# Optimization experiments

Measured on AMD Instinct MI355X. Metric: run time of the kernel, lower is better.

## Reference

```python
import jax, jax.numpy as jnp
import numpy as np

POOL_H, POOL_W = 7, 7
SCALE = 0.25
SAMPLING = 2  # fixed sampling ratio (static grid)


def _sample_coords(lo, bin_sz, pool, s):
    # lo: [N], bin_sz: [N] -> coords [N, pool*s]
    # point iy within bin: (iy + 0.5) / s of a bin
    offs = (jnp.arange(pool)[:, None] + (jnp.arange(s)[None, :] + 0.5) / s).reshape(-1)  # [pool*s]
    return lo[:, None] + offs[None, :] * bin_sz[:, None]


def roi_align(feat, rois, roibatches):
    B, C, H, W = feat.shape
    N = rois.shape[0]
    x1 = rois[:, 0] * SCALE
    y1 = rois[:, 1] * SCALE
    x2 = rois[:, 2] * SCALE
    y2 = rois[:, 3] * SCALE
    roi_w = jnp.maximum(x2 - x1, 1.0)
    roi_h = jnp.maximum(y2 - y1, 1.0)
    bin_w = roi_w / POOL_W
    bin_h = roi_h / POOL_H

    ys = _sample_coords(y1, bin_h, POOL_H, SAMPLING)  # [N, Gy]
    xs = _sample_coords(x1, bin_w, POOL_W, SAMPLING)  # [N, Gx]
    Gy, Gx = ys.shape[1], xs.shape[1]

    vy = (ys >= -1.0) & (ys <= H)  # out-of-range samples contribute 0
    vx = (xs >= -1.0) & (xs <= W)

    yc = jnp.clip(ys, 0.0, H - 1)
    xc = jnp.clip(xs, 0.0, W - 1)
    y_lo = jnp.clip(jnp.floor(yc).astype(jnp.int32), 0, H - 1)
    x_lo = jnp.clip(jnp.floor(xc).astype(jnp.int32), 0, W - 1)
    y_hi = jnp.minimum(y_lo + 1, H - 1)
    x_hi = jnp.minimum(x_lo + 1, W - 1)
    ly = yc - y_lo  # [N, Gy]
    lx = xc - x_lo  # [N, Gx]
    hy = 1.0 - ly
    hx = 1.0 - lx

    b = roibatches.astype(jnp.int32)[:, None, None]  # [N,1,1]

    def gather(yi, xi):
        # advanced indexing -> [N, Gy, Gx, C]
        return feat[b, :, yi[:, :, None], xi[:, None, :]]

    v_ll = gather(y_lo, x_lo)
    v_lh = gather(y_lo, x_hi)
    v_hl = gather(y_hi, x_lo)
    v_hh = gather(y_hi, x_hi)

    wy_l = (hy * vy)[:, :, None, None]
    wy_h = (ly * vy)[:, :, None, None]
    wx_l = (hx * vx)[:, None, :, None]
    wx_h = (lx * vx)[:, None, :, None]

    vals = (wy_l * wx_l * v_ll + wy_l * wx_h * v_lh
            + wy_h * wx_l * v_hl + wy_h * wx_h * v_hh)  # [N, Gy, Gx, C]

    # average pool over the SAMPLING x SAMPLING points per bin
    vals = vals.reshape(N, POOL_H, SAMPLING, POOL_W, SAMPLING, C)
    out = vals.mean(axis=(2, 4))  # [N, POOL_H, POOL_W, C]
    return jnp.transpose(out, (0, 3, 1, 2))  # [N, C, POOL_H, POOL_W]


def setup_inputs() -> dict:
    key = jax.random.key(0)
    k1, k2, k3, k4 = jax.random.split(key, 4)
    B, C, H, W = 4, 256, 200, 304
    N = 1024
    img_h, img_w = H / SCALE, W / SCALE
    feat = jax.random.normal(k1, (B, C, H, W), dtype=jnp.float32)
    xa = jax.random.uniform(k2, (N, 2), minval=0.0, maxval=img_w)
    ya = jax.random.uniform(k3, (N, 2), minval=0.0, maxval=img_h)
    rois = jnp.stack([xa.min(1), ya.min(1), xa.max(1), ya.max(1)], axis=1).astype(jnp.float32)
    roibatches = jax.random.randint(k4, (N,), 0, B, dtype=jnp.int32)
    return {"feat": feat, "rois": rois, "roibatches": roibatches}


def reference(feat, rois, roibatches):
    return roi_align(feat, rois, roibatches)
```

## Files before the change

kernel.cpp:

```cpp
#include <hip/hip_runtime.h>
#include <hip/hip_bf16.h>


#define POOL 7
constexpr int Bc = 4;
constexpr int Cc = 256;
constexpr int Hc = 200;
constexpr int Wc = 304;
constexpr int HWc = Hc * Wc;
constexpr float SCALEc = 0.25f;

static __device__ __forceinline__ float bf16_lo(unsigned u) {
    u <<= 16;
    return __builtin_bit_cast(float, u);
}
static __device__ __forceinline__ float bf16_hi(unsigned u) {
    u &= 0xFFFF0000u;
    return __builtin_bit_cast(float, u);
}

__global__ __launch_bounds__(256) void nchw_to_nhwc_bf16(
    const float* __restrict__ in, ushort* __restrict__ outp)
{
    __shared__ float tile[128][65];
    int b  = blockIdx.z;
    int p0 = blockIdx.x * 64;
    int c0 = blockIdx.y * 128;
    int tx = threadIdx.x;
    int ty = threadIdx.y;

    const float* src = in + ((size_t)b * Cc + c0) * (size_t)HWc + p0;
#pragma unroll
    for (int k = 0; k < 32; ++k) {
        int c = ty + 4 * k;
        tile[c][tx] = src[(size_t)c * HWc + tx];
    }
    __syncthreads();

#pragma unroll
    for (int k = 0; k < 16; ++k) {
        int p = ty + 4 * k;
        float f0 = tile[2 * tx][p];
        float f1 = tile[2 * tx + 1][p];
        unsigned u0 = (unsigned)__hip_bfloat16_raw(__float2bfloat16(f0)).x;
        unsigned u1 = (unsigned)__hip_bfloat16_raw(__float2bfloat16(f1)).x;
        unsigned packed = u0 | (u1 << 16);
        size_t d = ((size_t)b * HWc + p0 + p) * (size_t)Cc + c0 + 2 * tx;
        *(unsigned*)(outp + d) = packed;
    }
}

__global__ __launch_bounds__(256) void roialign_gather(
    const ushort* __restrict__ f,
    const float*  __restrict__ rois,
    const int*    __restrict__ rb,
    float*        __restrict__ out)
{
    __shared__ float stage[49 * 257];

    int n    = blockIdx.x;
    int t    = threadIdx.x;
    int wav  = t >> 6;
    int lane = t & 63;
    int half = lane >> 5;
    int sub  = lane & 31;

    float x1 = rois[n * 4 + 0] * SCALEc;
    float y1 = rois[n * 4 + 1] * SCALEc;
    float x2 = rois[n * 4 + 2] * SCALEc;
    float y2 = rois[n * 4 + 3] * SCALEc;
    int   b  = rb[n];

    float roi_w = fmaxf(x2 - x1, 1.0f);
    float roi_h = fmaxf(y2 - y1, 1.0f);
    float bin_w = roi_w * (1.0f / POOL);
    float bin_h = roi_h * (1.0f / POOL);

    const ushort* base = f + (size_t)b * ((size_t)HWc * Cc) + (size_t)sub * 8;

#pragma unroll 1
    for (int it = 0; it < 7; ++it) {
        int bin = it * 8 + wav * 2 + half;
        if (bin < 49) {
            int ph = bin / POOL;
            int pw = bin % POOL;

            int   yy[2][2];  float wy[2][2];
#pragma unroll
            for (int iy = 0; iy < 2; ++iy) {
                float y  = y1 + ((float)ph + ((float)iy + 0.5f) * 0.5f) * bin_h;
                bool  vy = (y >= -1.0f) && (y <= (float)Hc);
                float yc = fminf(fmaxf(y, 0.0f), (float)(Hc - 1));
                int   y_lo = (int)floorf(yc);
                int   y_hi = min(y_lo + 1, Hc - 1);
                float ly = yc - (float)y_lo;
                yy[iy][0] = y_lo;  yy[iy][1] = y_hi;
                wy[iy][0] = vy ? (1.0f - ly) : 0.0f;
                wy[iy][1] = vy ? ly : 0.0f;
            }
            int   xx[2][2];  float wx[2][2];
#pragma unroll
            for (int ix = 0; ix < 2; ++ix) {
                float x  = x1 + ((float)pw + ((float)ix + 0.5f) * 0.5f) * bin_w;
                bool  vx = (x >= -1.0f) && (x <= (float)Wc);
                float xc = fminf(fmaxf(x, 0.0f), (float)(Wc - 1));
                int   x_lo = (int)floorf(xc);
                int   x_hi = min(x_lo + 1, Wc - 1);
                float lx = xc - (float)x_lo;
                xx[ix][0] = x_lo;  xx[ix][1] = x_hi;
                wx[ix][0] = vx ? (1.0f - lx) : 0.0f;
                wx[ix][1] = vx ? lx : 0.0f;
            }

            float acc[8] = {0.f, 0.f, 0.f, 0.f, 0.f, 0.f, 0.f, 0.f};
#pragma unroll
            for (int iy = 0; iy < 2; ++iy) {
#pragma unroll
                for (int yl = 0; yl < 2; ++yl) {
                    const ushort* row = base + (size_t)yy[iy][yl] * ((size_t)Wc * Cc);
                    float wyv = wy[iy][yl];
#pragma unroll
                    for (int ix = 0; ix < 2; ++ix) {
#pragma unroll
                        for (int xl = 0; xl < 2; ++xl) {
                            float w = wyv * wx[ix][xl];
                            const uint4 v = *(const uint4*)(row + (size_t)xx[ix][xl] * Cc);
                            acc[0] = fmaf(w, bf16_lo(v.x), acc[0]);
                            acc[1] = fmaf(w, bf16_hi(v.x), acc[1]);
                            acc[2] = fmaf(w, bf16_lo(v.y), acc[2]);
                            acc[3] = fmaf(w, bf16_hi(v.y), acc[3]);
                            acc[4] = fmaf(w, bf16_lo(v.z), acc[4]);
                            acc[5] = fmaf(w, bf16_hi(v.z), acc[5]);
                            acc[6] = fmaf(w, bf16_lo(v.w), acc[6]);
                            acc[7] = fmaf(w, bf16_hi(v.w), acc[7]);
                        }
                    }
                }
            }
            float* sp = &stage[bin * 257 + sub * 8];
#pragma unroll
            for (int j = 0; j < 8; ++j) sp[j] = acc[j] * 0.25f;
        }
    }
    __syncthreads();

    float* obase = out + (size_t)n * (Cc * POOL * POOL);
#pragma unroll 1
    for (int k = 0; k < 49; ++k) {
        int flat = t + 256 * k;
        int c    = flat / 49;
        int bin  = flat - c * 49;
        obase[flat] = stage[bin * 257 + c];
    }
}

__global__ __launch_bounds__(256) void roialign_fwd(
    const float* __restrict__ feat,
    const float* __restrict__ rois,
    const int* __restrict__ roibatches,
    float* __restrict__ out,
    int total)
{
    int tid = blockIdx.x * blockDim.x + threadIdx.x;
    if (tid >= total) return;
    int n   = tid / (Cc * POOL * POOL);
    int rem = tid % (Cc * POOL * POOL);
    int c   = rem / (POOL * POOL);
    int bin = rem % (POOL * POOL);
    int ph  = bin / POOL;
    int pw  = bin % POOL;

    float x1 = rois[n * 4 + 0] * SCALEc;
    float y1 = rois[n * 4 + 1] * SCALEc;
    float x2 = rois[n * 4 + 2] * SCALEc;
    float y2 = rois[n * 4 + 3] * SCALEc;
    int   b  = roibatches[n];

    float roi_w = fmaxf(x2 - x1, 1.0f);
    float roi_h = fmaxf(y2 - y1, 1.0f);
    float bin_w = roi_w * (1.0f / POOL);
    float bin_h = roi_h * (1.0f / POOL);

    const float* fp = feat + (size_t)(b * Cc + c) * (size_t)HWc;

    float acc = 0.0f;
#pragma unroll
    for (int iy = 0; iy < 2; ++iy) {
        float y  = y1 + ((float)ph + ((float)iy + 0.5f) * 0.5f) * bin_h;
        bool  vy = (y >= -1.0f) && (y <= (float)Hc);
        float yc = fminf(fmaxf(y, 0.0f), (float)(Hc - 1));
        int   y_lo = (int)floorf(yc);
        int   y_hi = min(y_lo + 1, Hc - 1);
        float ly = yc - (float)y_lo;
        float hy = 1.0f - ly;
        float wyl = vy ? hy : 0.0f;
        float wyh = vy ? ly : 0.0f;
        const float* row_lo = fp + (size_t)y_lo * Wc;
        const float* row_hi = fp + (size_t)y_hi * Wc;
#pragma unroll
        for (int ix = 0; ix < 2; ++ix) {
            float x  = x1 + ((float)pw + ((float)ix + 0.5f) * 0.5f) * bin_w;
            bool  vx = (x >= -1.0f) && (x <= (float)Wc);
            float xc = fminf(fmaxf(x, 0.0f), (float)(Wc - 1));
            int   x_lo = (int)floorf(xc);
            int   x_hi = min(x_lo + 1, Wc - 1);
            float lx = xc - (float)x_lo;
            float hx = 1.0f - lx;
            float wxl = vx ? hx : 0.0f;
            float wxh = vx ? lx : 0.0f;
            acc += wyl * (wxl * row_lo[x_lo] + wxh * row_lo[x_hi])
                 + wyh * (wxl * row_hi[x_lo] + wxh * row_hi[x_hi]);
        }
    }
    out[tid] = acc * 0.25f;
}

extern "C" void kernel_launch(void* const* d_in, const int* in_sizes, int n_in,
                              void* d_out, int out_size, void* d_ws, size_t ws_size,
                              hipStream_t stream)
{
    const float* feat       = (const float*)d_in[0];
    const float* rois       = (const float*)d_in[1];
    const int*   roibatches = (const int*)d_in[2];
    float*       out        = (float*)d_out;
    int N = in_sizes[1] / 4;

    size_t need = (size_t)Bc * HWc * Cc * sizeof(ushort);
    if (ws_size >= need) {
        ushort* fbh = (ushort*)d_ws;
        dim3 tgrid(HWc / 64, Cc / 128, Bc);
        dim3 tblock(64, 4);
        nchw_to_nhwc_bf16<<<tgrid, tblock, 0, stream>>>(feat, fbh);

        roialign_gather<<<N, 256, 0, stream>>>(fbh, rois, roibatches, out);
    } else {
        int total = out_size;
        roialign_fwd<<<(total + 255) / 256, 256, 0, stream>>>(
            feat, rois, roibatches, out, total);
    }
}
```

Measured before the change: 129.4 us.

## Vectorize NHWC transpose stores, double gather block size, batch gather loads

The transpose kernel now writes 16-byte uint4 stores of eight packed bf16 channels instead of 4-byte stores, with an XOR swizzle on the shared tile to limit bank conflicts on the new read pattern. The gather kernel launches 512 threads per ROI so each wave handles fewer bins, and it issues all eight row loads for a sample row before the FMAs to expose more memory-level parallelism. The cost is more registers held per thread and a bounds check in the output copy loop.

```diff
diff --git a/kernel.cpp b/kernel.cpp
--- a/kernel.cpp
+++ b/kernel.cpp
@@ -18,6 +18,11 @@
     u &= 0xFFFF0000u;
     return __builtin_bit_cast(float, u);
 }
+static __device__ __forceinline__ unsigned pack_bf16(float f0, float f1) {
+    unsigned u0 = (unsigned)__hip_bfloat16_raw(__float2bfloat16(f0)).x;
+    unsigned u1 = (unsigned)__hip_bfloat16_raw(__float2bfloat16(f1)).x;
+    return u0 | (u1 << 16);
+}
 
 __global__ __launch_bounds__(256) void nchw_to_nhwc_bf16(
     const float* __restrict__ in, ushort* __restrict__ outp)
@@ -33,24 +38,31 @@
 #pragma unroll
     for (int k = 0; k < 32; ++k) {
         int c = ty + 4 * k;
-        tile[c][tx] = src[(size_t)c * HWc + tx];
+        tile[c][tx ^ ((c >> 5) & 3)] = src[(size_t)c * HWc + tx];
     }
     __syncthreads();
 
-#pragma unroll
-    for (int k = 0; k < 16; ++k) {
-        int p = ty + 4 * k;
-        float f0 = tile[2 * tx][p];
-        float f1 = tile[2 * tx + 1][p];
-        unsigned u0 = (unsigned)__hip_bfloat16_raw(__float2bfloat16(f0)).x;
-        unsigned u1 = (unsigned)__hip_bfloat16_raw(__float2bfloat16(f1)).x;
-        unsigned packed = u0 | (u1 << 16);
-        size_t d = ((size_t)b * HWc + p0 + p) * (size_t)Cc + c0 + 2 * tx;
-        *(unsigned*)(outp + d) = packed;
-    }
-}
-
-__global__ __launch_bounds__(256) void roialign_gather(
+    int t  = ty * 64 + tx;
+    int cg = t & 15;
+    int pi = t >> 4;
+#pragma unroll
+    for (int k = 0; k < 4; ++k) {
+        int p = pi + 16 * k;
+        unsigned u[4];
+#pragma unroll
+        for (int j = 0; j < 4; ++j) {
+            int ce = cg * 8 + 2 * j;
+            int co = ce + 1;
+            float f0 = tile[ce][p ^ ((ce >> 5) & 3)];
+            float f1 = tile[co][p ^ ((co >> 5) & 3)];
+            u[j] = pack_bf16(f0, f1);
+        }
+        size_t d = ((size_t)b * HWc + p0 + p) * (size_t)Cc + c0 + cg * 8;
+        *(uint4*)(outp + d) = make_uint4(u[0], u[1], u[2], u[3]);
+    }
+}
+
+__global__ __launch_bounds__(512) void roialign_gather(
     const ushort* __restrict__ f,
     const float*  __restrict__ rois,
     const int*    __restrict__ rb,
@@ -79,8 +91,8 @@
     const ushort* base = f + (size_t)b * ((size_t)HWc * Cc) + (size_t)sub * 8;
 
 #pragma unroll 1
-    for (int it = 0; it < 7; ++it) {
-        int bin = it * 8 + wav * 2 + half;
+    for (int it = 0; it < 4; ++it) {
+        int bin = it * 16 + wav * 2 + half;
         if (bin < 49) {
             int ph = bin / POOL;
             int pw = bin % POOL;
@@ -115,25 +127,31 @@
             float acc[8] = {0.f, 0.f, 0.f, 0.f, 0.f, 0.f, 0.f, 0.f};
 #pragma unroll
             for (int iy = 0; iy < 2; ++iy) {
+                uint4 v[2][4];
 #pragma unroll
                 for (int yl = 0; yl < 2; ++yl) {
                     const ushort* row = base + (size_t)yy[iy][yl] * ((size_t)Wc * Cc);
-                    float wyv = wy[iy][yl];
-#pragma unroll
-                    for (int ix = 0; ix < 2; ++ix) {
-#pragma unroll
-                        for (int xl = 0; xl < 2; ++xl) {
-                            float w = wyv * wx[ix][xl];
-                            const uint4 v = *(const uint4*)(row + (size_t)xx[ix][xl] * Cc);
-                            acc[0] = fmaf(w, bf16_lo(v.x), acc[0]);
-                            acc[1] = fmaf(w, bf16_hi(v.x), acc[1]);
-                            acc[2] = fmaf(w, bf16_lo(v.y), acc[2]);
-                            acc[3] = fmaf(w, bf16_hi(v.y), acc[3]);
-                            acc[4] = fmaf(w, bf16_lo(v.z), acc[4]);
-                            acc[5] = fmaf(w, bf16_hi(v.z), acc[5]);
-                            acc[6] = fmaf(w, bf16_lo(v.w), acc[6]);
-                            acc[7] = fmaf(w, bf16_hi(v.w), acc[7]);
-                        }
+#pragma unroll
+                    for (int q = 0; q < 4; ++q) {
+                        int ix = q >> 1, xl = q & 1;
+                        v[yl][q] = *(const uint4*)(row + (size_t)xx[ix][xl] * Cc);
+                    }
+                }
+#pragma unroll
+                for (int yl = 0; yl < 2; ++yl) {
+#pragma unroll
+                    for (int q = 0; q < 4; ++q) {
+                        int ix = q >> 1, xl = q & 1;
+                        float w = wy[iy][yl] * wx[ix][xl];
+                        const uint4 vv = v[yl][q];
+                        acc[0] = fmaf(w, bf16_lo(vv.x), acc[0]);
+                        acc[1] = fmaf(w, bf16_hi(vv.x), acc[1]);
+                        acc[2] = fmaf(w, bf16_lo(vv.y), acc[2]);
+                        acc[3] = fmaf(w, bf16_hi(vv.y), acc[3]);
+                        acc[4] = fmaf(w, bf16_lo(vv.z), acc[4]);
+                        acc[5] = fmaf(w, bf16_hi(vv.z), acc[5]);
+                        acc[6] = fmaf(w, bf16_lo(vv.w), acc[6]);
+                        acc[7] = fmaf(w, bf16_hi(vv.w), acc[7]);
                     }
                 }
             }
@@ -146,11 +164,13 @@
 
     float* obase = out + (size_t)n * (Cc * POOL * POOL);
 #pragma unroll 1
-    for (int k = 0; k < 49; ++k) {
-        int flat = t + 256 * k;
-        int c    = flat / 49;
-        int bin  = flat - c * 49;
-        obase[flat] = stage[bin * 257 + c];
+    for (int k = 0; k < 25; ++k) {
+        int flat = t + 512 * k;
+        if (flat < Cc * POOL * POOL) {
+            int c   = flat / 49;
+            int bin = flat - c * 49;
+            obase[flat] = stage[bin * 257 + c];
+        }
     }
 }
 
@@ -232,7 +252,7 @@
         dim3 tblock(64, 4);
         nchw_to_nhwc_bf16<<<tgrid, tblock, 0, stream>>>(feat, fbh);
 
-        roialign_gather<<<N, 256, 0, stream>>>(fbh, rois, roibatches, out);
+        roialign_gather<<<N, 512, 0, stream>>>(fbh, rois, roibatches, out);
     } else {
         int total = out_size;
         roialign_fwd<<<(total + 255) / 256, 256, 0, stream>>>(
```

New measurement: 124.1 us. 4.1% less time.
